# Performance work log

Measured on AMD Instinct MI355X. Metric: run time of the kernel, lower is better.

## Reference

```python
import jax, jax.numpy as jnp
import numpy as np

B, T, D, H, O = 256, 512, 256, 1024, 256


def _uniform(key, shape, fan_in):
    # kaiming_uniform with a=0.1: bound = sqrt(6 / ((1 + a^2) * fan_in))
    bound = float(np.sqrt(6.0 / ((1.0 + 0.1 ** 2) * fan_in)))
    return jax.random.uniform(key, shape, jnp.float32, -bound, bound)


def setup_inputs() -> dict:
    key = jax.random.key(0)
    ks = jax.random.split(key, 8)
    inp = {
        "x": jax.random.normal(ks[0], (B, T, D), jnp.float32),
        "W_gx": _uniform(ks[1], (D, H), D),
        "W_gh": _uniform(ks[2], (H, H), H),
        "b_g": jnp.zeros((H,), jnp.float32),
        "W_ix": _uniform(ks[3], (D, H), D),
        "W_ih": _uniform(ks[4], (H, H), H),
        "b_i": jnp.zeros((H,), jnp.float32),
        "W_fx": _uniform(ks[5], (D, H), D),
        "W_fh": _uniform(ks[6], (H, H), H),
        "b_f": jnp.zeros((H,), jnp.float32),
        "W_ox": _uniform(jax.random.fold_in(key, 10), (D, H), D),
        "W_oh": _uniform(jax.random.fold_in(key, 11), (H, H), H),
        "b_o": jnp.zeros((H,), jnp.float32),
        "W_ph": _uniform(ks[7], (H, O), H),
        "b_p": jnp.zeros((O,), jnp.float32),
    }
    return inp


def reference(x, W_gx, W_gh, b_g, W_ix, W_ih, b_i, W_fx, W_fh, b_f,
              W_ox, W_oh, b_o, W_ph, b_p):
    Hd = W_gh.shape[0]
    # Fuse the 4 per-gate matmuls into two GEMMs (same math as the loop).
    Wx = jnp.concatenate([W_gx, W_ix, W_fx, W_ox], axis=1)  # [D, 4H]
    Wh = jnp.concatenate([W_gh, W_ih, W_fh, W_oh], axis=1)  # [H, 4H]
    b = jnp.concatenate([b_g, b_i, b_f, b_o])               # [4H]
    xW = jnp.einsum('btd,dk->tbk', x, Wx) + b                # [T, B, 4H]

    def step(carry, xw_t):
        h, c = carry
        z = xw_t + h @ Wh                                    # [B, 4H]
        g = jnp.tanh(z[:, :Hd])
        i = jax.nn.sigmoid(z[:, Hd:2 * Hd])
        f = jax.nn.sigmoid(z[:, 2 * Hd:3 * Hd])
        o = jax.nn.sigmoid(z[:, 3 * Hd:])
        c = g * i + c * f
        h = jnp.tanh(c) * o
        return (h, c), None

    h0 = jnp.zeros((x.shape[0], Hd), x.dtype)
    (h, _), _ = jax.lax.scan(step, (h0, h0), xW)
    return jax.nn.softmax(h @ W_ph + b_p, axis=1)
```

## Files before the change

kernel.cpp:

```cpp
#include <hip/hip_runtime.h>


typedef _Float16 f16;
typedef _Float16 f16x8 __attribute__((ext_vector_type(8)));
typedef _Float16 f16x4 __attribute__((ext_vector_type(4)));
typedef float f32x4 __attribute__((ext_vector_type(4)));
typedef unsigned int u32;

#define WS_WT    0
#define WS_WPHT  10485760
#define WS_HBUF  11010048
#define WS_LG    12058624
#define WS_CNT   12320768
#define WS_TICK  12322816

#define ZB    81920u
#define BCAST 114688

__device__ __forceinline__ float sigm(float v) { return 1.0f / (1.0f + __expf(-v)); }
__device__ __forceinline__ float tanhfast(float v) {
  float t = __expf(-2.0f * fabsf(v));
  float r = (1.0f - t) / (1.0f + t);
  return v < 0.0f ? -r : r;
}

__global__ __launch_bounds__(256) void prep_wt(
    const float* __restrict__ Wgh, const float* __restrict__ Wih,
    const float* __restrict__ Wfh, const float* __restrict__ Woh,
    const float* __restrict__ Wgx, const float* __restrict__ Wix,
    const float* __restrict__ Wfx, const float* __restrict__ Wox,
    f16* __restrict__ WT)
{
  __shared__ float tile[32][33];
  int bid = blockIdx.x;
  int gate = bid / 1280;
  int rem  = bid % 1280;
  int jt = rem / 40, kt = rem % 40;
  const float* srcH = (gate==0)?Wgh:(gate==1)?Wih:(gate==2)?Wfh:Woh;
  const float* srcX = (gate==0)?Wgx:(gate==1)?Wix:(gate==2)?Wfx:Wox;
  const float* src = (kt < 32) ? (srcH + (size_t)(kt*32)*1024)
                               : (srcX + (size_t)(kt*32 - 1024)*1024);
  int t = threadIdx.x;
  {
    int jl = t & 31, kg = t >> 5;
#pragma unroll
    for (int it = 0; it < 4; ++it) {
      int kl = kg + it*8;
      tile[kl][jl] = src[(size_t)kl*1024 + jt*32 + jl];
    }
  }
  __syncthreads();
  {
    int kl = t & 31, jg = t >> 5;
#pragma unroll
    for (int it = 0; it < 4; ++it) {
      int jl2 = jg + it*8;
      WT[(size_t)(gate*1024 + jt*32 + jl2)*1280 + kt*32 + kl] = (f16)tile[kl][jl2];
    }
  }
}

__global__ __launch_bounds__(256) void prep_wph(const float* __restrict__ Wph,
                                                f16* __restrict__ WphT)
{
  __shared__ float tile[32][33];
  int bid = blockIdx.x;
  int jt = bid & 7, kt = bid >> 3;
  int t = threadIdx.x;
  {
    int jl = t & 31, kg = t >> 5;
#pragma unroll
    for (int it = 0; it < 4; ++it) {
      int kl = kg + it*8;
      tile[kl][jl] = Wph[(size_t)(kt*32 + kl)*256 + jt*32 + jl];
    }
  }
  __syncthreads();
  {
    int kl = t & 31, jg = t >> 5;
#pragma unroll
    for (int it = 0; it < 4; ++it) {
      int jl2 = jg + it*8;
      WphT[(size_t)(jt*32 + jl2)*1024 + kt*32 + kl] = (f16)tile[kl][jl2];
    }
  }
}

__global__ __launch_bounds__(512, 2) void lstm_main(
    const float* __restrict__ x, const f16* __restrict__ WT,
    const f16* __restrict__ WphT, f16* __restrict__ hbuf,
    const float* __restrict__ bgp, const float* __restrict__ bip,
    const float* __restrict__ bfp, const float* __restrict__ bop,
    const float* __restrict__ bpp, float* __restrict__ lg,
    u32* __restrict__ cnt, u32* __restrict__ tick, float* __restrict__ out)
{
  __shared__ __align__(16) char smem[114704];
  const int tid  = threadIdx.x;
  const int lane = tid & 63;
  const int wv   = tid >> 6;
  const int hgrp = wv & 1;
  const int kh   = wv >> 1;
  const int l15 = lane & 15, l4 = lane >> 4;

  u32 myxcd;
  asm volatile("s_getreg_b32 %0, hwreg(HW_REG_XCC_ID)" : "=s"(myxcd));
  myxcd &= 7u;
  if (tid == 0) {
    u32 t = __hip_atomic_fetch_add(tick + myxcd, 1u,
                                   __ATOMIC_RELAXED, __HIP_MEMORY_SCOPE_AGENT);
    *(volatile u32*)(smem + BCAST) = t;
  }
  if (wv == 0) {
    u32 v = 0;
    int guard = 0;
    for (;;) {
      v = (lane < 8) ? __hip_atomic_load(tick + lane, __ATOMIC_RELAXED,
                                         __HIP_MEMORY_SCOPE_AGENT) : 0u;
      u32 sum = v;
      sum += __shfl_xor(sum, 1);
      sum += __shfl_xor(sum, 2);
      sum += __shfl_xor(sum, 4);
      if (__shfl(sum, 0) == 256u) break;
      __builtin_amdgcn_s_sleep(1);
      if (++guard > (1 << 20)) break;
    }
    int even = __all((lane < 8) ? (v == 32u) : 1);
    if (lane == 0) *(volatile u32*)(smem + BCAST + 4) = (u32)even;
  }
  __syncthreads();
  const bool xloc = (*(volatile u32*)(smem + BCAST + 4)) != 0u;
  const u32 myticket = *(volatile u32*)(smem + BCAST);
  const int xg = xloc ? (int)myxcd    : (blockIdx.x & 7);
  const int cg = xloc ? (int)myticket : (blockIdx.x >> 3);
  u32* flg = cnt + xg*64;

  f16x8 Breg[10][4];
  {
    const int gate = l15 & 3, hsub = l15 >> 2;
#pragma unroll
    for (int f = 0; f < 4; ++f) {
      const int n = gate*1024 + cg*32 + hgrp*16 + f*4 + hsub;
      const f16* wb = WT + (size_t)n*1280 + kh*320 + l4*8;
#pragma unroll
      for (int kk = 0; kk < 10; ++kk) {
        Breg[kk][f] = *(const f16x8*)(wb + kk*32);
        asm volatile("" : "+v"(Breg[kk][f]));
      }
    }
  }

  const int bcol = cg*32 + (tid & 31);
  const float bgr = bgp[bcol], bir = bip[bcol], bfr = bfp[bcol], bor = bop[bcol];

  const u32 aoff = (u32)l15*2560u + (u32)(kh*640 + l4*16);
  const u32 aswz = (u32)l15 << 4;
  const int srow = tid >> 5;
  const int sseg = tid & 31;
  const u32 swzr = (u32)srow << 4;

  float cA = 0.0f, cB = 0.0f;

  u32 pre = 0xFFFFFFFFu;
  bool preOK = false;

#pragma unroll 1
  for (int slot = 0; slot < 1024; ++slot) {
    const int T = slot & 1, s = slot >> 1;
    const u32 Abase = (u32)T * 40960u;
    u32* flgT = flg + T*32;
    const int grow = xg*32 + T*16 + srow;

    {
      const float* xsrc = x + ((size_t)grow*512 + (size_t)s)*256;
      float4 xv0 = *(const float4*)(xsrc + (sseg     )*4);
      float4 xv1 = *(const float4*)(xsrc + (sseg + 32)*4);
      f16x4 hv;
      hv[0] = (f16)xv0.x; hv[1] = (f16)xv0.y; hv[2] = (f16)xv0.z; hv[3] = (f16)xv0.w;
      *(f16x4*)(smem + Abase + ((srow*2560u + 2048u + 8u*(u32)(sseg     )) ^ swzr)) = hv;
      hv[0] = (f16)xv1.x; hv[1] = (f16)xv1.y; hv[2] = (f16)xv1.z; hv[3] = (f16)xv1.w;
      *(f16x4*)(smem + Abase + ((srow*2560u + 2048u + 8u*(u32)(sseg + 32)) ^ swzr)) = hv;
    }
    if (s > 0 && !preOK) {
      const u32 tgt = (u32)s;
      u32 v = tgt;
      int guard = 0;
      for (;;) {
        if (lane < 32)
          v = __hip_atomic_load(flgT + lane, __ATOMIC_RELAXED,
                                __HIP_MEMORY_SCOPE_AGENT);
        if (__all(v >= tgt)) break;
        __builtin_amdgcn_s_sleep(1);
        if (++guard > (1 << 18)) break;
      }
      if (lane == 0) {
        if (xloc) { asm volatile("buffer_inv sc0\n\ts_waitcnt vmcnt(0)" ::: "memory"); }
        else      { __threadfence(); }
      }
    }
    {
      const f16* hsrc = hbuf + (size_t)(s & 1)*262144 + (size_t)grow*1024;
#pragma unroll
      for (int j = 0; j < 4; ++j) {
        int chunk = sseg + 32*j;
        uint4 v = *(const uint4*)(hsrc + chunk*8);
        *(uint4*)(smem + Abase + ((srow*2560u + 16u*(u32)chunk) ^ swzr)) = v;
      }
    }
    __syncthreads();
    f32x4 acc0 = {}, acc1 = {}, acc2 = {}, acc3 = {};
#pragma unroll
    for (int kk = 0; kk < 10; ++kk) {
      f16x8 av = *(const f16x8*)(smem + Abase + ((aoff + (u32)kk*64u) ^ aswz));
      acc0 = __builtin_amdgcn_mfma_f32_16x16x32_f16(Breg[kk][0], av, acc0, 0, 0, 0);
      acc1 = __builtin_amdgcn_mfma_f32_16x16x32_f16(Breg[kk][1], av, acc1, 0, 0, 0);
      acc2 = __builtin_amdgcn_mfma_f32_16x16x32_f16(Breg[kk][2], av, acc2, 0, 0, 0);
      acc3 = __builtin_amdgcn_mfma_f32_16x16x32_f16(Breg[kk][3], av, acc3, 0, 0, 0);
    }
    {
      const int nT = (slot + 1) & 1, nS = (slot + 1) >> 1;
      pre = 0xFFFFFFFFu;
      if (nS > 0 && nS < 512 && lane < 32)
        pre = __hip_atomic_load(flg + nT*32 + lane, __ATOMIC_RELAXED,
                                __HIP_MEMORY_SCOPE_AGENT);
    }
    {
      const u32 zkh = ZB + (u32)kh*8192u;
#pragma unroll
      for (int f = 0; f < 4; ++f) {
        const u32 hcol = (u32)(hgrp*16 + f*4 + l4);
        const u32 s16 = ((u32)(l15*32) + hcol) ^ ((u32)(l15 & 7));
        f32x4 acc = (f==0)?acc0:(f==1)?acc1:(f==2)?acc2:acc3;
        *(f32x4*)(smem + zkh + s16*16u) = acc;
      }
    }
    __syncthreads();
    {
      f16* hw = hbuf + (size_t)((s & 1) ^ 1)*262144;
      const int row = tid >> 5, hcol = tid & 31;
      const u32 s16 = ((u32)(row*32) + (u32)hcol) ^ ((u32)(row & 7));
      const u32 ro = s16*16u;
      f32x4 z0 = *(const f32x4*)(smem + ZB +        ro);
      f32x4 z1 = *(const f32x4*)(smem + ZB + 8192u  + ro);
      f32x4 z2 = *(const f32x4*)(smem + ZB + 16384u + ro);
      f32x4 z3 = *(const f32x4*)(smem + ZB + 24576u + ro);
      float zg = z0[0] + z1[0] + z2[0] + z3[0] + bgr;
      float zi = z0[1] + z1[1] + z2[1] + z3[1] + bir;
      float zf = z0[2] + z1[2] + z2[2] + z3[2] + bfr;
      float zo = z0[3] + z1[3] + z2[3] + z3[3] + bor;
      float cv = T ? cB : cA;
      float gv = tanhfast(zg);
      float iv = sigm(zi);
      float fv = sigm(zf);
      float ov = sigm(zo);
      float cn = gv*iv + cv*fv;
      if (T) cB = cn; else cA = cn;
      hw[(size_t)(xg*32 + T*16 + row)*1024 + cg*32 + hcol] = (f16)(tanhfast(cn) * ov);
    }
    {
      const int nS = (slot + 1) >> 1;
      bool ok = (nS >= 512) || __all(pre >= (u32)nS);
      preOK = xloc && ok;
      if (preOK && nS < 512 && lane == 0) {
        asm volatile("buffer_inv sc0\n\ts_waitcnt vmcnt(0)" ::: "memory");
      }
    }
    __syncthreads();
    if (tid == 0) {
      if (!xloc) __threadfence();
      __hip_atomic_store(flgT + cg, (u32)(s + 1),
                         __ATOMIC_RELAXED, __HIP_MEMORY_SCOPE_AGENT);
    }
  }

  if (wv == 0) {
    u32 v = 512u;
    int guard = 0;
    for (;;) {
      v = __hip_atomic_load(flg + lane, __ATOMIC_RELAXED,
                            __HIP_MEMORY_SCOPE_AGENT);
      if (__all(v >= 512u)) break;
      __builtin_amdgcn_s_sleep(1);
      if (++guard > (1 << 18)) break;
    }
    if (lane == 0) {
      if (xloc) { asm volatile("buffer_inv sc0\n\ts_waitcnt vmcnt(0)" ::: "memory"); }
      else      { __threadfence(); }
    }
  }
  __syncthreads();
  {
#pragma unroll 1
    for (int p = 0; p < 32; ++p) {
      int rowl = wv*4 + (p >> 3);
      int oc   = p & 7;
      const f16* hp = hbuf + (size_t)(xg*32 + rowl)*1024 + lane*16;
      const f16* wp = WphT + (size_t)(cg*8 + oc)*1024 + lane*16;
      f16x8 h0 = *(const f16x8*)hp;
      f16x8 h1 = *(const f16x8*)(hp + 8);
      f16x8 w0 = *(const f16x8*)wp;
      f16x8 w1 = *(const f16x8*)(wp + 8);
      float sum = 0.f;
#pragma unroll
      for (int q = 0; q < 8; ++q)
        sum += (float)h0[q]*(float)w0[q] + (float)h1[q]*(float)w1[q];
#pragma unroll
      for (int d = 1; d < 64; d <<= 1) sum += __shfl_xor(sum, d);
      if (lane == 0)
        lg[(size_t)(xg*32 + rowl)*256 + cg*8 + oc] = sum + bpp[cg*8 + oc];
    }
  }
  __syncthreads();
  if (tid == 0) {
    if (!xloc) __threadfence();
    __hip_atomic_store(flg + cg, 513u, __ATOMIC_RELAXED, __HIP_MEMORY_SCOPE_AGENT);
  }
  if (wv == 0) {
    u32 v = 513u;
    int guard = 0;
    for (;;) {
      if (lane < 32)
        v = __hip_atomic_load(flg + lane, __ATOMIC_RELAXED, __HIP_MEMORY_SCOPE_AGENT);
      if (__all(v >= 513u)) break;
      __builtin_amdgcn_s_sleep(1);
      if (++guard > (1 << 18)) break;
    }
    if (lane == 0) {
      if (xloc) { asm volatile("buffer_inv sc0\n\ts_waitcnt vmcnt(0)" ::: "memory"); }
      else      { __threadfence(); }
    }
  }
  __syncthreads();
  if (tid < 64) {
    int rowg = xg*32 + cg;
    const float* lr = lg + (size_t)rowg*256;
    float v0 = lr[tid], v1 = lr[tid+64], v2 = lr[tid+128], v3 = lr[tid+192];
    float mx = fmaxf(fmaxf(v0, v1), fmaxf(v2, v3));
#pragma unroll
    for (int d = 1; d < 64; d <<= 1) mx = fmaxf(mx, __shfl_xor(mx, d));
    float e0 = __expf(v0-mx), e1 = __expf(v1-mx), e2 = __expf(v2-mx), e3 = __expf(v3-mx);
    float sm = e0+e1+e2+e3;
#pragma unroll
    for (int d = 1; d < 64; d <<= 1) sm += __shfl_xor(sm, d);
    float inv = 1.0f / sm;
    float* orow = out + (size_t)rowg*256;
    orow[tid]      = e0*inv;
    orow[tid+64]   = e1*inv;
    orow[tid+128]  = e2*inv;
    orow[tid+192]  = e3*inv;
  }
}

extern "C" void kernel_launch(void* const* d_in, const int* in_sizes, int n_in,
                              void* d_out, int out_size, void* d_ws, size_t ws_size,
                              hipStream_t stream) {
  (void)in_sizes; (void)n_in; (void)out_size; (void)ws_size;
  const float* x   = (const float*)d_in[0];
  const float* Wgx = (const float*)d_in[1];
  const float* Wgh = (const float*)d_in[2];
  const float* bg  = (const float*)d_in[3];
  const float* Wix = (const float*)d_in[4];
  const float* Wih = (const float*)d_in[5];
  const float* bi  = (const float*)d_in[6];
  const float* Wfx = (const float*)d_in[7];
  const float* Wfh = (const float*)d_in[8];
  const float* bf  = (const float*)d_in[9];
  const float* Wox = (const float*)d_in[10];
  const float* Woh = (const float*)d_in[11];
  const float* bo  = (const float*)d_in[12];
  const float* Wph = (const float*)d_in[13];
  const float* bp  = (const float*)d_in[14];

  char* ws = (char*)d_ws;
  f16*   WT   = (f16*)(ws + WS_WT);
  f16*   WphT = (f16*)(ws + WS_WPHT);
  f16*   hbuf = (f16*)(ws + WS_HBUF);
  float* lg   = (float*)(ws + WS_LG);
  u32*   cnt  = (u32*)(ws + WS_CNT);
  u32*   tick = (u32*)(ws + WS_TICK);

  hipMemsetAsync(hbuf, 0, 524288, stream);
  hipMemsetAsync(cnt, 0, 2048 + 64, stream);

  prep_wt<<<5120, 256, 0, stream>>>(Wgh, Wih, Wfh, Woh, Wgx, Wix, Wfx, Wox, WT);
  prep_wph<<<256, 256, 0, stream>>>(Wph, WphT);
  lstm_main<<<256, 512, 0, stream>>>(x, WT, WphT, hbuf,
                                     bg, bi, bf, bo, bp,
                                     lg, cnt, tick, (float*)d_out);
}
```

Baseline: 2.485 ms.

## Drop per-step block barriers via per-wave A loads and LDS counter flag publish

Each wave now loads exactly the h/x slice of the A tile it consumes, so the first __syncthreads per step becomes a wave-local lgkmcnt wait. The z staging buffer is double-buffered by parity, and the trailing block barrier is replaced by an LDS atomic counter: the last wave to finish publishes the global ready flag. When the workspace is large enough, x is also pre-converted to fp16 in a separate kernel, halving x traffic inside the recurrent loop. This adds an extra pass over x and raises LDS use to about 147KB. Visibility of other waves' hbuf writes now depends only on each wave's vmcnt wait before the counter increment.

```diff
diff --git a/kernel.cpp b/kernel.cpp
--- a/kernel.cpp
+++ b/kernel.cpp
@@ -13,9 +13,12 @@
 #define WS_LG    12058624
 #define WS_CNT   12320768
 #define WS_TICK  12322816
-
-#define ZB    81920u
-#define BCAST 114688
+#define WS_XH    16777216
+#define WS_XH_END 83886080
+
+#define ZBT   81920u
+#define CNTL  147456
+#define BCAST 147464
 
 __device__ __forceinline__ float sigm(float v) { return 1.0f / (1.0f + __expf(-v)); }
 __device__ __forceinline__ float tanhfast(float v) {
@@ -86,15 +89,30 @@
   }
 }
 
+__global__ __launch_bounds__(256) void prep_x16(const float* __restrict__ x,
+                                                f16* __restrict__ xh)
+{
+  size_t i = ((size_t)blockIdx.x*256 + threadIdx.x) * 16;
+  const float4* src = (const float4*)(x + i);
+  f16x4* dst = (f16x4*)(xh + i);
+#pragma unroll
+  for (int j = 0; j < 4; ++j) {
+    float4 v = src[j];
+    f16x4 h; h[0]=(f16)v.x; h[1]=(f16)v.y; h[2]=(f16)v.z; h[3]=(f16)v.w;
+    dst[j] = h;
+  }
+}
+
 __global__ __launch_bounds__(512, 2) void lstm_main(
-    const float* __restrict__ x, const f16* __restrict__ WT,
-    const f16* __restrict__ WphT, f16* __restrict__ hbuf,
+    const float* __restrict__ x, const f16* __restrict__ xh, int use_xh,
+    const f16* __restrict__ WT, const f16* __restrict__ WphT,
+    f16* __restrict__ hbuf,
     const float* __restrict__ bgp, const float* __restrict__ bip,
     const float* __restrict__ bfp, const float* __restrict__ bop,
     const float* __restrict__ bpp, float* __restrict__ lg,
     u32* __restrict__ cnt, u32* __restrict__ tick, float* __restrict__ out)
 {
-  __shared__ __align__(16) char smem[114704];
+  __shared__ __align__(16) char smem[147472];
   const int tid  = threadIdx.x;
   const int lane = tid & 63;
   const int wv   = tid >> 6;
@@ -106,6 +124,8 @@
   asm volatile("s_getreg_b32 %0, hwreg(HW_REG_XCC_ID)" : "=s"(myxcd));
   myxcd &= 7u;
   if (tid == 0) {
+    ((u32*)(smem + CNTL))[0] = 0u;
+    ((u32*)(smem + CNTL))[1] = 0u;
     u32 t = __hip_atomic_fetch_add(tick + myxcd, 1u,
                                    __ATOMIC_RELAXED, __HIP_MEMORY_SCOPE_AGENT);
     *(volatile u32*)(smem + BCAST) = t;
@@ -154,9 +174,9 @@
 
   const u32 aoff = (u32)l15*2560u + (u32)(kh*640 + l4*16);
   const u32 aswz = (u32)l15 << 4;
-  const int srow = tid >> 5;
-  const int sseg = tid & 31;
-  const u32 swzr = (u32)srow << 4;
+  const int r16 = lane & 15;
+  const int c4  = lane >> 4;
+  const u32 sswz = (u32)r16 << 4;
 
   float cA = 0.0f, cB = 0.0f;
 
@@ -167,18 +187,36 @@
   for (int slot = 0; slot < 1024; ++slot) {
     const int T = slot & 1, s = slot >> 1;
     const u32 Abase = (u32)T * 40960u;
+    const u32 Zt = ZBT + (u32)T * 32768u;
     u32* flgT = flg + T*32;
-    const int grow = xg*32 + T*16 + srow;
-
-    {
-      const float* xsrc = x + ((size_t)grow*512 + (size_t)s)*256;
-      float4 xv0 = *(const float4*)(xsrc + (sseg     )*4);
-      float4 xv1 = *(const float4*)(xsrc + (sseg + 32)*4);
-      f16x4 hv;
-      hv[0] = (f16)xv0.x; hv[1] = (f16)xv0.y; hv[2] = (f16)xv0.z; hv[3] = (f16)xv0.w;
-      *(f16x4*)(smem + Abase + ((srow*2560u + 2048u + 8u*(u32)(sseg     )) ^ swzr)) = hv;
-      hv[0] = (f16)xv1.x; hv[1] = (f16)xv1.y; hv[2] = (f16)xv1.z; hv[3] = (f16)xv1.w;
-      *(f16x4*)(smem + Abase + ((srow*2560u + 2048u + 8u*(u32)(sseg + 32)) ^ swzr)) = hv;
+    const int gT = xg*32 + T*16 + r16;
+
+    if (kh == 3) {
+      if (use_xh) {
+        const char* xrow = (const char*)xh + ((size_t)gT*512 + (size_t)s)*512;
+#pragma unroll
+        for (int j = 0; j < 10; ++j) {
+          int cc = c4 + 4*j;
+          if (cc >= 8) {
+            uint4 v = *(const uint4*)(xrow + (cc - 8)*16);
+            *(uint4*)(smem + Abase + (((u32)r16*2560u + (u32)(1920 + cc*16)) ^ sswz)) = v;
+          }
+        }
+      } else {
+        const float* xrowf = x + ((size_t)gT*512 + (size_t)s)*256;
+#pragma unroll
+        for (int j = 0; j < 10; ++j) {
+          int cc = c4 + 4*j;
+          if (cc >= 8) {
+            const float* p = xrowf + (cc - 8)*8;
+            float4 a = *(const float4*)p, b = *(const float4*)(p + 4);
+            f16x8 hv;
+            hv[0]=(f16)a.x; hv[1]=(f16)a.y; hv[2]=(f16)a.z; hv[3]=(f16)a.w;
+            hv[4]=(f16)b.x; hv[5]=(f16)b.y; hv[6]=(f16)b.z; hv[7]=(f16)b.w;
+            *(f16x8*)(smem + Abase + (((u32)r16*2560u + (u32)(1920 + cc*16)) ^ sswz)) = hv;
+          }
+        }
+      }
     }
     if (s > 0 && !preOK) {
       const u32 tgt = (u32)s;
@@ -198,15 +236,19 @@
       }
     }
     {
-      const f16* hsrc = hbuf + (size_t)(s & 1)*262144 + (size_t)grow*1024;
-#pragma unroll
-      for (int j = 0; j < 4; ++j) {
-        int chunk = sseg + 32*j;
-        uint4 v = *(const uint4*)(hsrc + chunk*8);
-        *(uint4*)(smem + Abase + ((srow*2560u + 16u*(u32)chunk) ^ swzr)) = v;
-      }
-    }
-    __syncthreads();
+      const char* hrow = (const char*)hbuf + (size_t)(s & 1)*524288
+                       + (size_t)gT*2048;
+#pragma unroll
+      for (int j = 0; j < 10; ++j) {
+        int cc = c4 + 4*j;
+        if (!(kh == 3 && cc >= 8)) {
+          uint4 v = *(const uint4*)(hrow + kh*640 + cc*16);
+          *(uint4*)(smem + Abase + (((u32)r16*2560u + (u32)(kh*640 + cc*16)) ^ sswz)) = v;
+        }
+      }
+    }
+    asm volatile("s_waitcnt lgkmcnt(0)" ::: "memory");
+    __builtin_amdgcn_sched_barrier(0);
     f32x4 acc0 = {}, acc1 = {}, acc2 = {}, acc3 = {};
 #pragma unroll
     for (int kk = 0; kk < 10; ++kk) {
@@ -224,7 +266,7 @@
                                 __HIP_MEMORY_SCOPE_AGENT);
     }
     {
-      const u32 zkh = ZB + (u32)kh*8192u;
+      const u32 zkh = Zt + (u32)kh*8192u;
 #pragma unroll
       for (int f = 0; f < 4; ++f) {
         const u32 hcol = (u32)(hgrp*16 + f*4 + l4);
@@ -239,10 +281,10 @@
       const int row = tid >> 5, hcol = tid & 31;
       const u32 s16 = ((u32)(row*32) + (u32)hcol) ^ ((u32)(row & 7));
       const u32 ro = s16*16u;
-      f32x4 z0 = *(const f32x4*)(smem + ZB +        ro);
-      f32x4 z1 = *(const f32x4*)(smem + ZB + 8192u  + ro);
-      f32x4 z2 = *(const f32x4*)(smem + ZB + 16384u + ro);
-      f32x4 z3 = *(const f32x4*)(smem + ZB + 24576u + ro);
+      f32x4 z0 = *(const f32x4*)(smem + Zt +          ro);
+      f32x4 z1 = *(const f32x4*)(smem + Zt + 8192u  + ro);
+      f32x4 z2 = *(const f32x4*)(smem + Zt + 16384u + ro);
+      f32x4 z3 = *(const f32x4*)(smem + Zt + 24576u + ro);
       float zg = z0[0] + z1[0] + z2[0] + z3[0] + bgr;
       float zi = z0[1] + z1[1] + z2[1] + z3[1] + bir;
       float zf = z0[2] + z1[2] + z2[2] + z3[2] + bfr;
@@ -256,6 +298,15 @@
       if (T) cB = cn; else cA = cn;
       hw[(size_t)(xg*32 + T*16 + row)*1024 + cg*32 + hcol] = (f16)(tanhfast(cn) * ov);
     }
+    asm volatile("s_waitcnt vmcnt(0)" ::: "memory");
+    if (lane == 0) {
+      u32 old = atomicAdd((u32*)(smem + CNTL) + T, 1u);
+      if (old == (u32)(8*s + 7)) {
+        if (!xloc) __threadfence();
+        __hip_atomic_store(flgT + cg, (u32)(s + 1),
+                           __ATOMIC_RELAXED, __HIP_MEMORY_SCOPE_AGENT);
+      }
+    }
     {
       const int nS = (slot + 1) >> 1;
       bool ok = (nS >= 512) || __all(pre >= (u32)nS);
@@ -263,12 +314,6 @@
       if (preOK && nS < 512 && lane == 0) {
         asm volatile("buffer_inv sc0\n\ts_waitcnt vmcnt(0)" ::: "memory");
       }
-    }
-    __syncthreads();
-    if (tid == 0) {
-      if (!xloc) __threadfence();
-      __hip_atomic_store(flgT + cg, (u32)(s + 1),
-                         __ATOMIC_RELAXED, __HIP_MEMORY_SCOPE_AGENT);
     }
   }
 
@@ -353,7 +398,7 @@
 extern "C" void kernel_launch(void* const* d_in, const int* in_sizes, int n_in,
                               void* d_out, int out_size, void* d_ws, size_t ws_size,
                               hipStream_t stream) {
-  (void)in_sizes; (void)n_in; (void)out_size; (void)ws_size;
+  (void)in_sizes; (void)n_in; (void)out_size;
   const float* x   = (const float*)d_in[0];
   const float* Wgx = (const float*)d_in[1];
   const float* Wgh = (const float*)d_in[2];
@@ -377,13 +422,17 @@
   float* lg   = (float*)(ws + WS_LG);
   u32*   cnt  = (u32*)(ws + WS_CNT);
   u32*   tick = (u32*)(ws + WS_TICK);
+  const int use_xh = (ws_size >= (size_t)WS_XH_END) ? 1 : 0;
+  f16*   xh   = (f16*)(ws + WS_XH);
 
   hipMemsetAsync(hbuf, 0, 524288, stream);
   hipMemsetAsync(cnt, 0, 2048 + 64, stream);
 
   prep_wt<<<5120, 256, 0, stream>>>(Wgh, Wih, Wfh, Woh, Wgx, Wix, Wfx, Wox, WT);
   prep_wph<<<256, 256, 0, stream>>>(Wph, WphT);
-  lstm_main<<<256, 512, 0, stream>>>(x, WT, WphT, hbuf,
+  if (use_xh)
+    prep_x16<<<8192, 256, 0, stream>>>(x, xh);
+  lstm_main<<<256, 512, 0, stream>>>(x, xh, use_xh, WT, WphT, hbuf,
                                      bg, bi, bf, bo, bp,
                                      lg, cnt, tick, (float*)d_out);
 }
```

Measured after the change: 4.558 ms. 83.4% more time.
